# Optimization experiments

Measured on AMD Instinct MI355X. Metric: run time of the kernel, lower is better.

The kernel has to match this reference:

```python
import jax, jax.numpy as jnp
import numpy as np

B, L, V, A = 4096, 64, 50000, 1000
E, H, G, F2 = 32, 32, 256, 512


def _xavier(k, shape):
    fan_out, fan_in = shape
    a = np.sqrt(6.0 / (fan_in + fan_out)).astype(np.float32)
    return jax.random.uniform(k, shape, jnp.float32, -a, a)


def setup_inputs() -> dict:
    key = jax.random.key(0)
    ks = jax.random.split(key, 32)
    inp = {}
    inp["q"] = jax.random.randint(ks[0], (B, L), 0, V)
    for i in range(8):
        inp[f"sf{i}"] = jax.random.randint(ks[1 + i], (B, L), 0, V)
    inp["emb"] = _xavier(ks[9], (V, E))
    # torch LSTM weight layout: [4H, in] with gate order i,f,g,o; biases init to 0
    inp["q_Wih"] = _xavier(ks[10], (4 * H, E))
    inp["q_Whh"] = _xavier(ks[11], (4 * H, H))
    inp["q_b"] = jnp.zeros((4 * H,), jnp.float32)
    inp["sf_Wih"] = _xavier(ks[12], (4 * H, E))
    inp["sf_Whh"] = _xavier(ks[13], (4 * H, H))
    inp["sf_b"] = jnp.zeros((4 * H,), jnp.float32)
    inp["g1_W"] = _xavier(ks[14], (G, 2 * H + 1)); inp["g1_b"] = jnp.zeros((G,), jnp.float32)
    inp["g2_W"] = _xavier(ks[15], (G, G)); inp["g2_b"] = jnp.zeros((G,), jnp.float32)
    inp["g3_W"] = _xavier(ks[16], (G, G)); inp["g3_b"] = jnp.zeros((G,), jnp.float32)
    inp["g4_W"] = _xavier(ks[17], (G, G)); inp["g4_b"] = jnp.zeros((G,), jnp.float32)
    inp["f1_W"] = _xavier(ks[18], (G, G)); inp["f1_b"] = jnp.zeros((G,), jnp.float32)
    inp["f2_W"] = _xavier(ks[19], (F2, G)); inp["f2_b"] = jnp.zeros((F2,), jnp.float32)
    inp["f3_W"] = _xavier(ks[20], (A, F2)); inp["f3_b"] = jnp.zeros((A,), jnp.float32)
    return inp


def _lstm_last(x, Wih, Whh, b):
    """x: [L, N, E] -> final hidden state [N, H]. Torch gate order i,f,g,o."""
    n = x.shape[1]
    h_dim = Whh.shape[1]
    def step(carry, xt):
        h, c = carry
        gates = xt @ Wih.T + h @ Whh.T + b  # [N, 4H]
        i, f, g, o = jnp.split(gates, 4, axis=-1)
        c = jax.nn.sigmoid(f) * c + jax.nn.sigmoid(i) * jnp.tanh(g)
        h = jax.nn.sigmoid(o) * jnp.tanh(c)
        return (h, c), None
    init = (jnp.zeros((n, h_dim), x.dtype), jnp.zeros((n, h_dim), x.dtype))
    (h, _), _ = jax.lax.scan(step, init, x)
    return h


def _lin(x, W, b):
    return x @ W.T + b


def reference(q, sf0, sf1, sf2, sf3, sf4, sf5, sf6, sf7,
              emb, q_Wih, q_Whh, q_b, sf_Wih, sf_Whh, sf_b,
              g1_W, g1_b, g2_W, g2_b, g3_W, g3_b, g4_W, g4_b,
              f1_W, f1_b, f2_W, f2_b, f3_W, f3_b):
    # dropout in eval mode (identity)
    b, l = q.shape
    qe = emb[q].transpose(1, 0, 2)  # [L, B, E]
    hq = _lstm_last(qe, q_Wih, q_Whh, q_b)  # [B, H]

    sf = jnp.stack([sf0, sf1, sf2, sf3, sf4, sf5, sf6, sf7])  # [8, B, L]
    sfe = emb[sf]  # [8, B, L, E]
    sfe = sfe.transpose(2, 0, 1, 3).reshape(l, 8 * b, emb.shape[1])  # one fused LSTM over 8*B
    hs = _lstm_last(sfe, sf_Wih, sf_Whh, sf_b).reshape(8, b, -1)  # [8, B, H]

    pos = jnp.broadcast_to(jnp.arange(8, dtype=hs.dtype)[:, None, None], (8, b, 1))
    x = jnp.concatenate([hs, jnp.broadcast_to(hq, (8, b, hq.shape[-1])), pos], axis=-1)  # [8, B, 65]
    x = jax.nn.relu(_lin(x, g1_W, g1_b))
    x = jax.nn.relu(_lin(x, g2_W, g2_b))
    x = jax.nn.relu(_lin(x, g3_W, g3_b))
    x = jax.nn.relu(_lin(x, g4_W, g4_b))
    g_o = x.sum(axis=0)  # [B, 256] segment-sum over the 8 relations

    x = jax.nn.relu(_lin(g_o, f1_W, f1_b))
    x = jax.nn.relu(_lin(x, f2_W, f2_b))
    return _lin(x, f3_W, f3_b)  # [B, A]
```

## Files before the change

### kernel.cpp

```cpp
#include <hip/hip_runtime.h>
#include <stdint.h>
#include <stddef.h>

typedef __fp16 f16;
typedef __attribute__((ext_vector_type(8))) __fp16 half8;
typedef __attribute__((ext_vector_type(4))) float f32x4;

static __device__ __forceinline__ f32x4 mfma16(half8 a, half8 b, f32x4 c) {
    return __builtin_amdgcn_mfma_f32_16x16x32_f16(a, b, c, 0, 0, 0);
}
static __device__ __forceinline__ float fexp2(float x) { float r; asm("v_exp_f32 %0, %1" : "=v"(r) : "v"(x)); return r; }
static __device__ __forceinline__ float frcp(float x)  { float r; asm("v_rcp_f32 %0, %1" : "=v"(r) : "v"(x)); return r; }

static constexpr float L2E  = 1.4426950408889634f;
static constexpr float L2E2 = 2.8853900817779268f;

static constexpr size_t OFF_EMB   = 0;
static constexpr size_t OFF_WQIH  = 3200000;
static constexpr size_t OFF_WQHH  = OFF_WQIH + 8192;
static constexpr size_t OFF_WSIH  = OFF_WQHH + 8192;
static constexpr size_t OFF_WSHH  = OFF_WSIH + 8192;
static constexpr size_t OFF_BQ    = OFF_WSHH + 8192;
static constexpr size_t OFF_BS    = OFF_BQ + 512;
static constexpr size_t OFF_G1WP  = OFF_BS + 512;
static constexpr size_t OFF_BIAS8 = OFF_G1WP + 32768;
static constexpr size_t OFF_G2W   = OFF_BIAS8 + 8192;
static constexpr size_t OFF_G3W   = OFF_G2W + 131072;
static constexpr size_t OFF_G4W   = OFF_G3W + 131072;
static constexpr size_t OFF_F1W   = OFF_G4W + 131072;
static constexpr size_t OFF_F2W   = OFF_F1W + 131072;
static constexpr size_t OFF_F3W   = OFF_F2W + 262144;
static constexpr size_t OFF_HS    = OFF_F3W + 1024000;
static constexpr size_t OFF_HQ    = OFF_HS + 2097152;
static constexpr size_t OFF_ACT1  = OFF_HQ + 262144;
static constexpr size_t OFF_ACT2  = OFF_ACT1 + 16777216;
static constexpr size_t WS_NEED   = OFF_ACT2 + 16777216;
static constexpr size_t OFF_GO    = OFF_ACT1;
static constexpr size_t OFF_FA    = OFF_ACT1 + 2097152;
static constexpr size_t OFF_FB    = OFF_ACT1 + 4194304;

struct CvtJobs { const float* src[7]; f16* dst[7]; int n[7]; };

__global__ __launch_bounds__(256) void cvt_multi(CvtJobs j) {
    int t = blockIdx.y;
    int i = (blockIdx.x * 256 + threadIdx.x) * 8;
    if (i >= j.n[t]) return;
    const float* s = j.src[t] + i;
    f32x4 a = *(const f32x4*)s;
    f32x4 b = *(const f32x4*)(s + 4);
    half8 o;
    o[0]=(f16)a[0]; o[1]=(f16)a[1]; o[2]=(f16)a[2]; o[3]=(f16)a[3];
    o[4]=(f16)b[0]; o[5]=(f16)b[1]; o[6]=(f16)b[2]; o[7]=(f16)b[3];
    *(half8*)(j.dst[t] + i) = o;
}

__global__ __launch_bounds__(256) void prep_small(
    const float* __restrict__ g1W, const float* __restrict__ g1b,
    f16* __restrict__ wp, float* __restrict__ bias8,
    const float* __restrict__ qWih, const float* __restrict__ qWhh, const float* __restrict__ qb,
    const float* __restrict__ sWih, const float* __restrict__ sWhh, const float* __restrict__ sb,
    f16* __restrict__ wqih, f16* __restrict__ wqhh, float* __restrict__ bq,
    f16* __restrict__ wsih, f16* __restrict__ wshh, float* __restrict__ bs)
{
    int t = threadIdx.x;
    if (blockIdx.x == 0) {
        int col = t;
        for (int k = 0; k < 64; k++) wp[col * 64 + k] = (f16)g1W[col * 65 + k];
        float wpos = g1W[col * 65 + 64];
        float b = g1b[col];
        for (int i = 0; i < 8; i++) bias8[i * 256 + col] = b + (float)i * wpos;
    } else {
        for (int i = t; i < 4096; i += 256) {
            int row = i >> 5;
            float s = (row < 64 || row >= 96) ? -L2E : L2E2;
            wqih[i] = (f16)(qWih[i] * s);
            wqhh[i] = (f16)(qWhh[i] * s);
            wsih[i] = (f16)(sWih[i] * s);
            wshh[i] = (f16)(sWhh[i] * s);
        }
        if (t < 128) {
            float s = (t < 64 || t >= 96) ? -L2E : L2E2;
            bq[t] = qb[t] * s;
            bs[t] = sb[t] * s;
        }
    }
}

struct SfPtrs { const int* p[8]; };

__global__ __launch_bounds__(64) void lstm_kernel(
    SfPtrs sf, const int* __restrict__ qtok, const f16* __restrict__ emb_h,
    const f16* __restrict__ wih_sf, const f16* __restrict__ whh_sf, const float* __restrict__ b_sf,
    const f16* __restrict__ wih_q,  const f16* __restrict__ whh_q,  const float* __restrict__ b_q,
    f16* __restrict__ hs_out, f16* __restrict__ hq_out)
{
    __shared__ __align__(16) char hb[16 * 80];
    int lane = threadIdx.x;
    int c15 = lane & 15, kq = lane >> 4;
    int sbase = blockIdx.x * 16;
    bool isq = sbase >= 32768;
    const f16* wih = isq ? wih_q : wih_sf;
    const f16* whh = isq ? whh_q : whh_sf;
    const float* bvec = isq ? b_q : b_sf;

    half8 wi[8], wh[8];
    f32x4 bc[8];
    #pragma unroll
    for (int n = 0; n < 8; n++) {
        int col = n * 16 + c15;
        wi[n] = *(const half8*)(wih + col * 32 + kq * 8);
        wh[n] = *(const half8*)(whh + col * 32 + kq * 8);
        float b = bvec[col];
        bc[n][0] = b; bc[n][1] = b; bc[n][2] = b; bc[n][3] = b;
    }
    int sg = sbase + c15;
    const int* tp;
    if (isq) tp = qtok + (sg - 32768) * 64;
    else     tp = sf.p[sg >> 12] + (sg & 4095) * 64;

    f32x4 zro = {0.f, 0.f, 0.f, 0.f};
    *(f32x4*)(hb + lane * 16) = zro;
    if (lane < 16) *(f32x4*)(hb + 1024 + lane * 16) = zro;
    asm volatile("s_waitcnt lgkmcnt(0)" ::: "memory");

    float cst[4][2] = {};
    const char* hrd = hb + c15 * 80 + kq * 16;

    int tok = tp[0];
    half8 xf = *(const half8*)(emb_h + (size_t)tok * 32 + kq * 8);

    #pragma unroll 1
    for (int t = 0; t < 64; t++) {
        half8 hf = *(const half8*)hrd;
        f32x4 acc[8];
        #pragma unroll
        for (int n = 0; n < 8; n++) acc[n] = mfma16(xf, wi[n], bc[n]);
        #pragma unroll
        for (int n = 0; n < 8; n++) acc[n] = mfma16(hf, wh[n], acc[n]);
        if (t < 63) {
            int tk = tp[t + 1];
            xf = *(const half8*)(emb_h + (size_t)tk * 32 + kq * 8);
        }
        #pragma unroll
        for (int r = 0; r < 4; r++) {
            #pragma unroll
            for (int jh = 0; jh < 2; jh++) {
                float ei = fexp2(acc[0 + jh][r]);
                float ef = fexp2(acc[2 + jh][r]);
                float eg = fexp2(acc[4 + jh][r]);
                float eo = fexp2(acc[6 + jh][r]);
                float si  = frcp(1.f + ei);
                float sfv = frcp(1.f + ef);
                float so  = frcp(1.f + eo);
                float tg  = fmaf(-2.f, frcp(1.f + eg), 1.f);
                float cn  = fmaf(sfv, cst[r][jh], si * tg);
                cst[r][jh] = cn;
                float e2  = fexp2(cn * L2E2);
                float th  = fmaf(-2.f, frcp(1.f + e2), 1.f);
                float hn  = so * th;
                *(f16*)(hb + (kq * 4 + r) * 80 + (jh * 16 + c15) * 2) = (f16)hn;
            }
        }
        asm volatile("s_waitcnt lgkmcnt(0)" ::: "memory");
    }
    int row = lane >> 2, ch = lane & 3;
    half8 hv = *(const half8*)(hb + row * 80 + ch * 16);
    int so_ = sbase + row;
    if (isq) *(half8*)(hq_out + (size_t)(so_ - 32768) * 32 + ch * 8) = hv;
    else     *(half8*)(hs_out + (size_t)so_ * 32 + ch * 8) = hv;
}

__global__ __launch_bounds__(256) void gemm_g1(
    const f16* __restrict__ hs, const f16* __restrict__ hq,
    const f16* __restrict__ Wp, const float* __restrict__ bias8,
    f16* __restrict__ out)
{
    int wave = threadIdx.x >> 6, lane = threadIdx.x & 63;
    int c15 = lane & 15, kq = lane >> 4;
    int wm = wave >> 1, wn = wave & 1;
    int m0 = blockIdx.x * 128 + wm * 64;
    int n0 = blockIdx.y * 128 + wn * 64;
    const float* bias = bias8 + ((blockIdx.x * 128) >> 12) * 256;
    f32x4 zro = {0.f, 0.f, 0.f, 0.f};
    f32x4 acc[4][4];
    #pragma unroll
    for (int a = 0; a < 4; a++)
        #pragma unroll
        for (int b = 0; b < 4; b++) acc[a][b] = zro;

    half8 av[4], bv[4];
    #pragma unroll
    for (int fm = 0; fm < 4; fm++) av[fm] = *(const half8*)(hs + (size_t)(m0 + fm * 16 + c15) * 32 + kq * 8);
    #pragma unroll
    for (int fn = 0; fn < 4; fn++) bv[fn] = *(const half8*)(Wp + (size_t)(n0 + fn * 16 + c15) * 64 + kq * 8);
    #pragma unroll
    for (int fm = 0; fm < 4; fm++)
        #pragma unroll
        for (int fn = 0; fn < 4; fn++) acc[fm][fn] = mfma16(av[fm], bv[fn], acc[fm][fn]);
    #pragma unroll
    for (int fm = 0; fm < 4; fm++) av[fm] = *(const half8*)(hq + (size_t)((m0 + fm * 16 + c15) & 4095) * 32 + kq * 8);
    #pragma unroll
    for (int fn = 0; fn < 4; fn++) bv[fn] = *(const half8*)(Wp + (size_t)(n0 + fn * 16 + c15) * 64 + 32 + kq * 8);
    #pragma unroll
    for (int fm = 0; fm < 4; fm++)
        #pragma unroll
        for (int fn = 0; fn < 4; fn++) acc[fm][fn] = mfma16(av[fm], bv[fn], acc[fm][fn]);
    #pragma unroll
    for (int fn = 0; fn < 4; fn++) {
        int col = n0 + fn * 16 + c15;
        float bb = bias[col];
        #pragma unroll
        for (int fm = 0; fm < 4; fm++)
            #pragma unroll
            for (int r = 0; r < 4; r++) {
                int row = m0 + fm * 16 + kq * 4 + r;
                float v = acc[fm][fn][r] + bb;
                v = fmaxf(v, 0.f);
                out[(size_t)row * 256 + col] = (f16)v;
            }
    }
}

template<int K, bool RELU, bool OUTF32>
__global__ __launch_bounds__(256) void gemm_k(
    const f16* __restrict__ A, const f16* __restrict__ W, const float* __restrict__ bias,
    void* __restrict__ outv, int N, int ldout)
{
    int wave = threadIdx.x >> 6, lane = threadIdx.x & 63;
    int c15 = lane & 15, kq = lane >> 4;
    int wm = wave >> 1, wn = wave & 1;
    int m0 = blockIdx.x * 128 + wm * 64;
    int n0 = blockIdx.y * 128 + wn * 64;
    f32x4 zro = {0.f, 0.f, 0.f, 0.f};
    f32x4 acc[4][4];
    #pragma unroll
    for (int a = 0; a < 4; a++)
        #pragma unroll
        for (int b = 0; b < 4; b++) acc[a][b] = zro;

    const f16* ap[4];
    const f16* bp[4];
    #pragma unroll
    for (int fm = 0; fm < 4; fm++) ap[fm] = A + (size_t)(m0 + fm * 16 + c15) * K + kq * 8;
    #pragma unroll
    for (int fn = 0; fn < 4; fn++) {
        int col = n0 + fn * 16 + c15;
        if (col > N - 1) col = N - 1;
        bp[fn] = W + (size_t)col * K + kq * 8;
    }
    for (int k0 = 0; k0 < K; k0 += 32) {
        half8 av[4], bv[4];
        #pragma unroll
        for (int fm = 0; fm < 4; fm++) av[fm] = *(const half8*)(ap[fm] + k0);
        #pragma unroll
        for (int fn = 0; fn < 4; fn++) bv[fn] = *(const half8*)(bp[fn] + k0);
        #pragma unroll
        for (int fm = 0; fm < 4; fm++)
            #pragma unroll
            for (int fn = 0; fn < 4; fn++) acc[fm][fn] = mfma16(av[fm], bv[fn], acc[fm][fn]);
    }
    #pragma unroll
    for (int fn = 0; fn < 4; fn++) {
        int col = n0 + fn * 16 + c15;
        if (col < N) {
            float bb = bias[col];
            #pragma unroll
            for (int fm = 0; fm < 4; fm++)
                #pragma unroll
                for (int r = 0; r < 4; r++) {
                    int row = m0 + fm * 16 + kq * 4 + r;
                    float v = acc[fm][fn][r] + bb;
                    if (RELU) v = fmaxf(v, 0.f);
                    if (OUTF32) ((float*)outv)[(size_t)row * ldout + col] = v;
                    else ((f16*)outv)[(size_t)row * ldout + col] = (f16)v;
                }
        }
    }
}

__global__ __launch_bounds__(256) void sum8_kernel(const f16* __restrict__ g4o, f16* __restrict__ go) {
    int t = blockIdx.x * 256 + threadIdx.x;
    int b = t >> 5, chk = t & 31;
    const f16* p = g4o + (size_t)b * 256 + chk * 8;
    float a[8] = {};
    #pragma unroll
    for (int i = 0; i < 8; i++) {
        half8 v = *(const half8*)(p + (size_t)i * 4096 * 256);
        #pragma unroll
        for (int j = 0; j < 8; j++) a[j] += (float)v[j];
    }
    half8 o;
    #pragma unroll
    for (int j = 0; j < 8; j++) o[j] = (f16)a[j];
    *(half8*)(go + (size_t)b * 256 + chk * 8) = o;
}

extern "C" void kernel_launch(void* const* d_in, const int* in_sizes, int n_in,
                              void* d_out, int out_size, void* d_ws, size_t ws_size,
                              hipStream_t stream)
{
    if (ws_size < WS_NEED) return;
    const int* q_tok = (const int*)d_in[0];
    SfPtrs sf;
    for (int i = 0; i < 8; i++) sf.p[i] = (const int*)d_in[1 + i];
    const float* emb_f = (const float*)d_in[9];
    const float* qWih = (const float*)d_in[10];
    const float* qWhh = (const float*)d_in[11];
    const float* q_b  = (const float*)d_in[12];
    const float* sWih = (const float*)d_in[13];
    const float* sWhh = (const float*)d_in[14];
    const float* s_b  = (const float*)d_in[15];
    const float* g1W  = (const float*)d_in[16];
    const float* g1b  = (const float*)d_in[17];
    const float* g2W  = (const float*)d_in[18];
    const float* g2b  = (const float*)d_in[19];
    const float* g3W  = (const float*)d_in[20];
    const float* g3b  = (const float*)d_in[21];
    const float* g4W  = (const float*)d_in[22];
    const float* g4b  = (const float*)d_in[23];
    const float* f1W  = (const float*)d_in[24];
    const float* f1b  = (const float*)d_in[25];
    const float* f2W  = (const float*)d_in[26];
    const float* f2b  = (const float*)d_in[27];
    const float* f3W  = (const float*)d_in[28];
    const float* f3b  = (const float*)d_in[29];

    char* ws = (char*)d_ws;
    f16* emb_h = (f16*)(ws + OFF_EMB);
    f16* wqih  = (f16*)(ws + OFF_WQIH);
    f16* wqhh  = (f16*)(ws + OFF_WQHH);
    f16* wsih  = (f16*)(ws + OFF_WSIH);
    f16* wshh  = (f16*)(ws + OFF_WSHH);
    float* bq  = (float*)(ws + OFF_BQ);
    float* bs  = (float*)(ws + OFF_BS);
    f16* g1wp  = (f16*)(ws + OFF_G1WP);
    float* bias8 = (float*)(ws + OFF_BIAS8);
    f16* g2w = (f16*)(ws + OFF_G2W);
    f16* g3w = (f16*)(ws + OFF_G3W);
    f16* g4w = (f16*)(ws + OFF_G4W);
    f16* f1w = (f16*)(ws + OFF_F1W);
    f16* f2w = (f16*)(ws + OFF_F2W);
    f16* f3w = (f16*)(ws + OFF_F3W);
    f16* hs  = (f16*)(ws + OFF_HS);
    f16* hq  = (f16*)(ws + OFF_HQ);
    f16* act1 = (f16*)(ws + OFF_ACT1);
    f16* act2 = (f16*)(ws + OFF_ACT2);
    f16* go = (f16*)(ws + OFF_GO);
    f16* fa = (f16*)(ws + OFF_FA);
    f16* fb = (f16*)(ws + OFF_FB);

    CvtJobs cj;
    const float* srcs[7] = {emb_f, g2W, g3W, g4W, f1W, f2W, f3W};
    f16* dsts[7]         = {emb_h, g2w, g3w, g4w, f1w, f2w, f3w};
    int ns[7] = {1600000, 65536, 65536, 65536, 65536, 131072, 512000};
    for (int i = 0; i < 7; i++) { cj.src[i] = srcs[i]; cj.dst[i] = dsts[i]; cj.n[i] = ns[i]; }

    cvt_multi<<<dim3(782, 7), 256, 0, stream>>>(cj);
    prep_small<<<2, 256, 0, stream>>>(g1W, g1b, g1wp, bias8,
                                      qWih, qWhh, q_b, sWih, sWhh, s_b,
                                      wqih, wqhh, bq, wsih, wshh, bs);
    lstm_kernel<<<2304, 64, 0, stream>>>(sf, q_tok, emb_h, wsih, wshh, bs, wqih, wqhh, bq, hs, hq);
    gemm_g1<<<dim3(256, 2), 256, 0, stream>>>(hs, hq, g1wp, bias8, act1);
    gemm_k<256, true, false><<<dim3(256, 2), 256, 0, stream>>>(act1, g2w, g2b, act2, 256, 256);
    gemm_k<256, true, false><<<dim3(256, 2), 256, 0, stream>>>(act2, g3w, g3b, act1, 256, 256);
    gemm_k<256, true, false><<<dim3(256, 2), 256, 0, stream>>>(act1, g4w, g4b, act2, 256, 256);
    sum8_kernel<<<512, 256, 0, stream>>>(act2, go);
    gemm_k<256, true, false><<<dim3(32, 2), 256, 0, stream>>>(go, f1w, f1b, fa, 256, 256);
    gemm_k<256, true, false><<<dim3(32, 4), 256, 0, stream>>>(fa, f2w, f2b, fb, 512, 512);
    gemm_k<512, false, true><<<dim3(32, 8), 256, 0, stream>>>(fb, f3w, f3b, d_out, 1000, 1000);
}
```

Baseline: 373.3 us.

## Fuse MLP layers into two kernels, transpose LSTM MFMA, merge prep kernels

Merges the conversion and prep kernels into one launch. Fuses g1 through g4 into a single kernel that keeps activations in shared memory, and fuses the 8-way sum with f1, f2 and f3 into a second kernel. This removes several launches and the HBM round trips for intermediate activations. The LSTM swaps MFMA operand order so each lane writes a contiguous half4 of h, and it rewrites the gate math to use fewer reciprocals. It also drops the explicit LDS waitcnt barriers, which risks synchronization hazards, and the fused GEMMs use smaller tiles that reload weights from global memory per block.

```diff
diff --git a/kernel.cpp b/kernel.cpp
--- a/kernel.cpp
+++ b/kernel.cpp
@@ -4,6 +4,7 @@
 
 typedef __fp16 f16;
 typedef __attribute__((ext_vector_type(8))) __fp16 half8;
+typedef __attribute__((ext_vector_type(4))) __fp16 half4;
 typedef __attribute__((ext_vector_type(4))) float f32x4;
 
 static __device__ __forceinline__ f32x4 mfma16(half8 a, half8 b, f32x4 c) {
@@ -14,6 +15,9 @@
 
 static constexpr float L2E  = 1.4426950408889634f;
 static constexpr float L2E2 = 2.8853900817779268f;
+
+static constexpr int LD256 = 280;
+static constexpr int LD512 = 536;
 
 static constexpr size_t OFF_EMB   = 0;
 static constexpr size_t OFF_WQIH  = 3200000;
@@ -32,29 +36,13 @@
 static constexpr size_t OFF_F3W   = OFF_F2W + 262144;
 static constexpr size_t OFF_HS    = OFF_F3W + 1024000;
 static constexpr size_t OFF_HQ    = OFF_HS + 2097152;
-static constexpr size_t OFF_ACT1  = OFF_HQ + 262144;
-static constexpr size_t OFF_ACT2  = OFF_ACT1 + 16777216;
+static constexpr size_t OFF_ACT2  = OFF_HQ + 262144;
 static constexpr size_t WS_NEED   = OFF_ACT2 + 16777216;
-static constexpr size_t OFF_GO    = OFF_ACT1;
-static constexpr size_t OFF_FA    = OFF_ACT1 + 2097152;
-static constexpr size_t OFF_FB    = OFF_ACT1 + 4194304;
 
 struct CvtJobs { const float* src[7]; f16* dst[7]; int n[7]; };
 
-__global__ __launch_bounds__(256) void cvt_multi(CvtJobs j) {
-    int t = blockIdx.y;
-    int i = (blockIdx.x * 256 + threadIdx.x) * 8;
-    if (i >= j.n[t]) return;
-    const float* s = j.src[t] + i;
-    f32x4 a = *(const f32x4*)s;
-    f32x4 b = *(const f32x4*)(s + 4);
-    half8 o;
-    o[0]=(f16)a[0]; o[1]=(f16)a[1]; o[2]=(f16)a[2]; o[3]=(f16)a[3];
-    o[4]=(f16)b[0]; o[5]=(f16)b[1]; o[6]=(f16)b[2]; o[7]=(f16)b[3];
-    *(half8*)(j.dst[t] + i) = o;
-}
-
-__global__ __launch_bounds__(256) void prep_small(
+__global__ __launch_bounds__(256) void cvt_prep(
+    CvtJobs j,
     const float* __restrict__ g1W, const float* __restrict__ g1b,
     f16* __restrict__ wp, float* __restrict__ bias8,
     const float* __restrict__ qWih, const float* __restrict__ qWhh, const float* __restrict__ qb,
@@ -63,13 +51,26 @@
     f16* __restrict__ wsih, f16* __restrict__ wshh, float* __restrict__ bs)
 {
     int t = threadIdx.x;
+    if (blockIdx.y < 7) {
+        int jb = blockIdx.y;
+        int i = (blockIdx.x * 256 + t) * 8;
+        if (i >= j.n[jb]) return;
+        const float* s = j.src[jb] + i;
+        f32x4 a = *(const f32x4*)s;
+        f32x4 b = *(const f32x4*)(s + 4);
+        half8 o;
+        o[0]=(f16)a[0]; o[1]=(f16)a[1]; o[2]=(f16)a[2]; o[3]=(f16)a[3];
+        o[4]=(f16)b[0]; o[5]=(f16)b[1]; o[6]=(f16)b[2]; o[7]=(f16)b[3];
+        *(half8*)(j.dst[jb] + i) = o;
+        return;
+    }
     if (blockIdx.x == 0) {
         int col = t;
         for (int k = 0; k < 64; k++) wp[col * 64 + k] = (f16)g1W[col * 65 + k];
         float wpos = g1W[col * 65 + 64];
         float b = g1b[col];
         for (int i = 0; i < 8; i++) bias8[i * 256 + col] = b + (float)i * wpos;
-    } else {
+    } else if (blockIdx.x == 1) {
         for (int i = t; i < 4096; i += 256) {
             int row = i >> 5;
             float s = (row < 64 || row >= 96) ? -L2E : L2E2;
@@ -107,11 +108,9 @@
     f32x4 bc[8];
     #pragma unroll
     for (int n = 0; n < 8; n++) {
-        int col = n * 16 + c15;
-        wi[n] = *(const half8*)(wih + col * 32 + kq * 8);
-        wh[n] = *(const half8*)(whh + col * 32 + kq * 8);
-        float b = bvec[col];
-        bc[n][0] = b; bc[n][1] = b; bc[n][2] = b; bc[n][3] = b;
+        wi[n] = *(const half8*)(wih + (n * 16 + c15) * 32 + kq * 8);
+        wh[n] = *(const half8*)(whh + (n * 16 + c15) * 32 + kq * 8);
+        bc[n] = *(const f32x4*)(bvec + n * 16 + kq * 4);
     }
     int sg = sbase + c15;
     const int* tp;
@@ -121,9 +120,8 @@
     f32x4 zro = {0.f, 0.f, 0.f, 0.f};
     *(f32x4*)(hb + lane * 16) = zro;
     if (lane < 16) *(f32x4*)(hb + 1024 + lane * 16) = zro;
-    asm volatile("s_waitcnt lgkmcnt(0)" ::: "memory");
-
-    float cst[4][2] = {};
+
+    float cst[2][4] = {};
     const char* hrd = hb + c15 * 80 + kq * 16;
 
     int tok = tp[0];
@@ -134,165 +132,240 @@
         half8 hf = *(const half8*)hrd;
         f32x4 acc[8];
         #pragma unroll
-        for (int n = 0; n < 8; n++) acc[n] = mfma16(xf, wi[n], bc[n]);
-        #pragma unroll
-        for (int n = 0; n < 8; n++) acc[n] = mfma16(hf, wh[n], acc[n]);
+        for (int n = 0; n < 8; n++) acc[n] = mfma16(wi[n], xf, bc[n]);
+        #pragma unroll
+        for (int n = 0; n < 8; n++) acc[n] = mfma16(wh[n], hf, acc[n]);
         if (t < 63) {
             int tk = tp[t + 1];
             xf = *(const half8*)(emb_h + (size_t)tk * 32 + kq * 8);
         }
         #pragma unroll
-        for (int r = 0; r < 4; r++) {
-            #pragma unroll
-            for (int jh = 0; jh < 2; jh++) {
+        for (int jh = 0; jh < 2; jh++) {
+            half4 hp;
+            #pragma unroll
+            for (int r = 0; r < 4; r++) {
                 float ei = fexp2(acc[0 + jh][r]);
                 float ef = fexp2(acc[2 + jh][r]);
                 float eg = fexp2(acc[4 + jh][r]);
                 float eo = fexp2(acc[6 + jh][r]);
-                float si  = frcp(1.f + ei);
-                float sfv = frcp(1.f + ef);
-                float so  = frcp(1.f + eo);
-                float tg  = fmaf(-2.f, frcp(1.f + eg), 1.f);
-                float cn  = fmaf(sfv, cst[r][jh], si * tg);
-                cst[r][jh] = cn;
-                float e2  = fexp2(cn * L2E2);
-                float th  = fmaf(-2.f, frcp(1.f + e2), 1.f);
-                float hn  = so * th;
-                *(f16*)(hb + (kq * 4 + r) * 80 + (jh * 16 + c15) * 2) = (f16)hn;
-            }
-        }
-        asm volatile("s_waitcnt lgkmcnt(0)" ::: "memory");
-    }
-    int row = lane >> 2, ch = lane & 3;
-    half8 hv = *(const half8*)(hb + row * 80 + ch * 16);
-    int so_ = sbase + row;
-    if (isq) *(half8*)(hq_out + (size_t)(so_ - 32768) * 32 + ch * 8) = hv;
-    else     *(half8*)(hs_out + (size_t)so_ * 32 + ch * 8) = hv;
-}
-
-__global__ __launch_bounds__(256) void gemm_g1(
-    const f16* __restrict__ hs, const f16* __restrict__ hq,
-    const f16* __restrict__ Wp, const float* __restrict__ bias8,
-    f16* __restrict__ out)
-{
-    int wave = threadIdx.x >> 6, lane = threadIdx.x & 63;
-    int c15 = lane & 15, kq = lane >> 4;
-    int wm = wave >> 1, wn = wave & 1;
-    int m0 = blockIdx.x * 128 + wm * 64;
-    int n0 = blockIdx.y * 128 + wn * 64;
-    const float* bias = bias8 + ((blockIdx.x * 128) >> 12) * 256;
-    f32x4 zro = {0.f, 0.f, 0.f, 0.f};
-    f32x4 acc[4][4];
+                float t1 = 1.f + ei, t2 = 1.f + ef, t5 = 1.f + eo;
+                float eg1 = eg + 1.f, egm = eg - 1.f;
+                float num = fmaf(egm, t2, cst[jh][r] * t1 * eg1);
+                float den = (t2 * t1) * eg1;
+                float cn  = num * frcp(den);
+                cst[jh][r] = cn;
+                float ec  = fexp2(cn * L2E2);
+                float hv  = (ec - 1.f) * frcp((ec + 1.f) * t5);
+                hp[r] = (f16)hv;
+            }
+            *(half4*)(hb + c15 * 80 + jh * 32 + kq * 8) = hp;
+        }
+    }
+    half8 hv = *(const half8*)hrd;
+    if (isq) *(half8*)(hq_out + (size_t)(sg - 32768) * 32 + kq * 8) = hv;
+    else     *(half8*)(hs_out + (size_t)sg * 32 + kq * 8) = hv;
+}
+
+template<bool TOGLOBAL>
+static __device__ __forceinline__ void layer256(
+    const f16 (* __restrict__ src)[LD256], f16 (* __restrict__ dst)[LD256],
+    const f16* __restrict__ W, const float* __restrict__ bias,
+    f16* __restrict__ gout, int m0, int wv, int c15, int kq)
+{
+    f32x4 acc[2][4];
     #pragma unroll
-    for (int a = 0; a < 4; a++)
-        #pragma unroll
-        for (int b = 0; b < 4; b++) acc[a][b] = zro;
-
-    half8 av[4], bv[4];
+    for (int a = 0; a < 2; a++)
+        #pragma unroll
+        for (int b = 0; b < 4; b++) acc[a][b] = (f32x4){0.f, 0.f, 0.f, 0.f};
     #pragma unroll
-    for (int fm = 0; fm < 4; fm++) av[fm] = *(const half8*)(hs + (size_t)(m0 + fm * 16 + c15) * 32 + kq * 8);
-    #pragma unroll
-    for (int fn = 0; fn < 4; fn++) bv[fn] = *(const half8*)(Wp + (size_t)(n0 + fn * 16 + c15) * 64 + kq * 8);
-    #pragma unroll
-    for (int fm = 0; fm < 4; fm++)
-        #pragma unroll
-        for (int fn = 0; fn < 4; fn++) acc[fm][fn] = mfma16(av[fm], bv[fn], acc[fm][fn]);
-    #pragma unroll
-    for (int fm = 0; fm < 4; fm++) av[fm] = *(const half8*)(hq + (size_t)((m0 + fm * 16 + c15) & 4095) * 32 + kq * 8);
-    #pragma unroll
-    for (int fn = 0; fn < 4; fn++) bv[fn] = *(const half8*)(Wp + (size_t)(n0 + fn * 16 + c15) * 64 + 32 + kq * 8);
-    #pragma unroll
-    for (int fm = 0; fm < 4; fm++)
-        #pragma unroll
-        for (int fn = 0; fn < 4; fn++) acc[fm][fn] = mfma16(av[fm], bv[fn], acc[fm][fn]);
+    for (int k0 = 0; k0 < 8; k0++) {
+        half8 av[2], bv[4];
+        #pragma unroll
+        for (int fm = 0; fm < 2; fm++) av[fm] = *(const half8*)(&src[fm * 16 + c15][k0 * 32 + kq * 8]);
+        #pragma unroll
+        for (int fn = 0; fn < 4; fn++) bv[fn] = *(const half8*)(W + (size_t)(wv * 64 + fn * 16 + c15) * 256 + k0 * 32 + kq * 8);
+        #pragma unroll
+        for (int fm = 0; fm < 2; fm++)
+            #pragma unroll
+            for (int fn = 0; fn < 4; fn++) acc[fm][fn] = mfma16(av[fm], bv[fn], acc[fm][fn]);
+    }
     #pragma unroll
     for (int fn = 0; fn < 4; fn++) {
-        int col = n0 + fn * 16 + c15;
+        int col = wv * 64 + fn * 16 + c15;
         float bb = bias[col];
         #pragma unroll
-        for (int fm = 0; fm < 4; fm++)
+        for (int fm = 0; fm < 2; fm++)
             #pragma unroll
             for (int r = 0; r < 4; r++) {
-                int row = m0 + fm * 16 + kq * 4 + r;
-                float v = acc[fm][fn][r] + bb;
-                v = fmaxf(v, 0.f);
-                out[(size_t)row * 256 + col] = (f16)v;
-            }
-    }
-}
-
-template<int K, bool RELU, bool OUTF32>
-__global__ __launch_bounds__(256) void gemm_k(
-    const f16* __restrict__ A, const f16* __restrict__ W, const float* __restrict__ bias,
-    void* __restrict__ outv, int N, int ldout)
-{
-    int wave = threadIdx.x >> 6, lane = threadIdx.x & 63;
-    int c15 = lane & 15, kq = lane >> 4;
-    int wm = wave >> 1, wn = wave & 1;
-    int m0 = blockIdx.x * 128 + wm * 64;
-    int n0 = blockIdx.y * 128 + wn * 64;
-    f32x4 zro = {0.f, 0.f, 0.f, 0.f};
-    f32x4 acc[4][4];
-    #pragma unroll
-    for (int a = 0; a < 4; a++)
-        #pragma unroll
-        for (int b = 0; b < 4; b++) acc[a][b] = zro;
-
-    const f16* ap[4];
-    const f16* bp[4];
-    #pragma unroll
-    for (int fm = 0; fm < 4; fm++) ap[fm] = A + (size_t)(m0 + fm * 16 + c15) * K + kq * 8;
-    #pragma unroll
-    for (int fn = 0; fn < 4; fn++) {
-        int col = n0 + fn * 16 + c15;
-        if (col > N - 1) col = N - 1;
-        bp[fn] = W + (size_t)col * K + kq * 8;
-    }
-    for (int k0 = 0; k0 < K; k0 += 32) {
-        half8 av[4], bv[4];
-        #pragma unroll
-        for (int fm = 0; fm < 4; fm++) av[fm] = *(const half8*)(ap[fm] + k0);
-        #pragma unroll
-        for (int fn = 0; fn < 4; fn++) bv[fn] = *(const half8*)(bp[fn] + k0);
-        #pragma unroll
-        for (int fm = 0; fm < 4; fm++)
+                float v = fmaxf(acc[fm][fn][r] + bb, 0.f);
+                if (TOGLOBAL) gout[(size_t)(m0 + fm * 16 + kq * 4 + r) * 256 + col] = (f16)v;
+                else          dst[fm * 16 + kq * 4 + r][col] = (f16)v;
+            }
+    }
+}
+
+__global__ __launch_bounds__(256) void gemm_g1234(
+    const f16* __restrict__ hs, const f16* __restrict__ hq,
+    const f16* __restrict__ g1wp, const float* __restrict__ bias8,
+    const f16* __restrict__ g2w, const float* __restrict__ g2b,
+    const f16* __restrict__ g3w, const float* __restrict__ g3b,
+    const f16* __restrict__ g4w, const float* __restrict__ g4b,
+    f16* __restrict__ act2)
+{
+    __shared__ __align__(16) f16 actA[32][LD256];
+    __shared__ __align__(16) f16 actB[32][LD256];
+    const int wv = threadIdx.x >> 6, lane = threadIdx.x & 63;
+    const int c15 = lane & 15, kq = lane >> 4;
+    const int m0 = blockIdx.x * 32;
+    const float* brow = bias8 + ((m0 >> 12) << 8);
+
+    {
+        f32x4 acc[2][4];
+        #pragma unroll
+        for (int a = 0; a < 2; a++)
+            #pragma unroll
+            for (int b = 0; b < 4; b++) acc[a][b] = (f32x4){0.f, 0.f, 0.f, 0.f};
+        half8 av[2], bv[4];
+        #pragma unroll
+        for (int fm = 0; fm < 2; fm++) av[fm] = *(const half8*)(hs + (size_t)(m0 + fm * 16 + c15) * 32 + kq * 8);
+        #pragma unroll
+        for (int fn = 0; fn < 4; fn++) bv[fn] = *(const half8*)(g1wp + (size_t)(wv * 64 + fn * 16 + c15) * 64 + kq * 8);
+        #pragma unroll
+        for (int fm = 0; fm < 2; fm++)
             #pragma unroll
             for (int fn = 0; fn < 4; fn++) acc[fm][fn] = mfma16(av[fm], bv[fn], acc[fm][fn]);
-    }
-    #pragma unroll
-    for (int fn = 0; fn < 4; fn++) {
-        int col = n0 + fn * 16 + c15;
-        if (col < N) {
-            float bb = bias[col];
-            #pragma unroll
-            for (int fm = 0; fm < 4; fm++)
+        #pragma unroll
+        for (int fm = 0; fm < 2; fm++) av[fm] = *(const half8*)(hq + (size_t)((m0 + fm * 16 + c15) & 4095) * 32 + kq * 8);
+        #pragma unroll
+        for (int fn = 0; fn < 4; fn++) bv[fn] = *(const half8*)(g1wp + (size_t)(wv * 64 + fn * 16 + c15) * 64 + 32 + kq * 8);
+        #pragma unroll
+        for (int fm = 0; fm < 2; fm++)
+            #pragma unroll
+            for (int fn = 0; fn < 4; fn++) acc[fm][fn] = mfma16(av[fm], bv[fn], acc[fm][fn]);
+        #pragma unroll
+        for (int fn = 0; fn < 4; fn++) {
+            int col = wv * 64 + fn * 16 + c15;
+            float bb = brow[col];
+            #pragma unroll
+            for (int fm = 0; fm < 2; fm++)
                 #pragma unroll
-                for (int r = 0; r < 4; r++) {
-                    int row = m0 + fm * 16 + kq * 4 + r;
-                    float v = acc[fm][fn][r] + bb;
-                    if (RELU) v = fmaxf(v, 0.f);
-                    if (OUTF32) ((float*)outv)[(size_t)row * ldout + col] = v;
-                    else ((f16*)outv)[(size_t)row * ldout + col] = (f16)v;
-                }
-        }
-    }
-}
-
-__global__ __launch_bounds__(256) void sum8_kernel(const f16* __restrict__ g4o, f16* __restrict__ go) {
-    int t = blockIdx.x * 256 + threadIdx.x;
-    int b = t >> 5, chk = t & 31;
-    const f16* p = g4o + (size_t)b * 256 + chk * 8;
-    float a[8] = {};
-    #pragma unroll
-    for (int i = 0; i < 8; i++) {
-        half8 v = *(const half8*)(p + (size_t)i * 4096 * 256);
-        #pragma unroll
-        for (int j = 0; j < 8; j++) a[j] += (float)v[j];
-    }
-    half8 o;
-    #pragma unroll
-    for (int j = 0; j < 8; j++) o[j] = (f16)a[j];
-    *(half8*)(go + (size_t)b * 256 + chk * 8) = o;
+                for (int r = 0; r < 4; r++)
+                    actA[fm * 16 + kq * 4 + r][col] = (f16)fmaxf(acc[fm][fn][r] + bb, 0.f);
+        }
+    }
+    __syncthreads();
+    layer256<false>(actA, actB, g2w, g2b, nullptr, m0, wv, c15, kq);
+    __syncthreads();
+    layer256<false>(actB, actA, g3w, g3b, nullptr, m0, wv, c15, kq);
+    __syncthreads();
+    layer256<true>(actA, actB, g4w, g4b, act2, m0, wv, c15, kq);
+}
+
+__global__ __launch_bounds__(256) void f123s_kernel(
+    const f16* __restrict__ act2,
+    const f16* __restrict__ f1w, const float* __restrict__ f1b,
+    const f16* __restrict__ f2w, const float* __restrict__ f2b,
+    const f16* __restrict__ f3w, const float* __restrict__ f3b,
+    float* __restrict__ out)
+{
+    __shared__ __align__(16) f16 smbuf[16][LD256];
+    __shared__ __align__(16) f16 f1buf[16][LD256];
+    __shared__ __align__(16) f16 f2buf[16][LD512];
+    const int b0 = blockIdx.x * 16;
+
+    {
+        int r = threadIdx.x >> 4, cb = (threadIdx.x & 15) * 16;
+        float s[16] = {};
+        #pragma unroll
+        for (int i = 0; i < 8; i++) {
+            const f16* p = act2 + ((size_t)(i * 4096 + b0 + r)) * 256 + cb;
+            half8 v0 = *(const half8*)p;
+            half8 v1 = *(const half8*)(p + 8);
+            #pragma unroll
+            for (int q = 0; q < 8; q++) { s[q] += (float)v0[q]; s[8 + q] += (float)v1[q]; }
+        }
+        half8 o0, o1;
+        #pragma unroll
+        for (int q = 0; q < 8; q++) { o0[q] = (f16)s[q]; o1[q] = (f16)s[8 + q]; }
+        *(half8*)(&smbuf[r][cb]) = o0;
+        *(half8*)(&smbuf[r][cb + 8]) = o1;
+    }
+    __syncthreads();
+    const int wv = threadIdx.x >> 6, lane = threadIdx.x & 63;
+    const int c15 = lane & 15, kq = lane >> 4;
+
+    {
+        f32x4 acc[4];
+        #pragma unroll
+        for (int b = 0; b < 4; b++) acc[b] = (f32x4){0.f, 0.f, 0.f, 0.f};
+        #pragma unroll
+        for (int k0 = 0; k0 < 8; k0++) {
+            half8 a = *(const half8*)(&smbuf[c15][k0 * 32 + kq * 8]);
+            #pragma unroll
+            for (int fn = 0; fn < 4; fn++) {
+                half8 bv = *(const half8*)(f1w + (size_t)(wv * 64 + fn * 16 + c15) * 256 + k0 * 32 + kq * 8);
+                acc[fn] = mfma16(a, bv, acc[fn]);
+            }
+        }
+        #pragma unroll
+        for (int fn = 0; fn < 4; fn++) {
+            int col = wv * 64 + fn * 16 + c15;
+            float bb = f1b[col];
+            #pragma unroll
+            for (int r = 0; r < 4; r++)
+                f1buf[kq * 4 + r][col] = (f16)fmaxf(acc[fn][r] + bb, 0.f);
+        }
+    }
+    __syncthreads();
+    {
+        f32x4 acc[8];
+        #pragma unroll
+        for (int b = 0; b < 8; b++) acc[b] = (f32x4){0.f, 0.f, 0.f, 0.f};
+        #pragma unroll
+        for (int k0 = 0; k0 < 8; k0++) {
+            half8 a = *(const half8*)(&f1buf[c15][k0 * 32 + kq * 8]);
+            #pragma unroll
+            for (int fn = 0; fn < 8; fn++) {
+                half8 bv = *(const half8*)(f2w + (size_t)(wv * 128 + fn * 16 + c15) * 256 + k0 * 32 + kq * 8);
+                acc[fn] = mfma16(a, bv, acc[fn]);
+            }
+        }
+        #pragma unroll
+        for (int fn = 0; fn < 8; fn++) {
+            int col = wv * 128 + fn * 16 + c15;
+            float bb = f2b[col];
+            #pragma unroll
+            for (int r = 0; r < 4; r++)
+                f2buf[kq * 4 + r][col] = (f16)fmaxf(acc[fn][r] + bb, 0.f);
+        }
+    }
+    __syncthreads();
+    {
+        f32x4 acc[16];
+        #pragma unroll
+        for (int b = 0; b < 16; b++) acc[b] = (f32x4){0.f, 0.f, 0.f, 0.f};
+        #pragma unroll
+        for (int k0 = 0; k0 < 16; k0++) {
+            half8 a = *(const half8*)(&f2buf[c15][k0 * 32 + kq * 8]);
+            #pragma unroll
+            for (int jj = 0; jj < 16; jj++) {
+                int col = (wv + 4 * jj) * 16 + c15;
+                int cl = col < 1000 ? col : 999;
+                half8 bv = *(const half8*)(f3w + (size_t)cl * 512 + k0 * 32 + kq * 8);
+                acc[jj] = mfma16(a, bv, acc[jj]);
+            }
+        }
+        #pragma unroll
+        for (int jj = 0; jj < 16; jj++) {
+            int col = (wv + 4 * jj) * 16 + c15;
+            if (col < 1000) {
+                float bb = f3b[col];
+                #pragma unroll
+                for (int r = 0; r < 4; r++)
+                    out[(size_t)(b0 + kq * 4 + r) * 1000 + col] = acc[jj][r] + bb;
+            }
+        }
+    }
 }
 
 extern "C" void kernel_launch(void* const* d_in, const int* in_sizes, int n_in,
@@ -343,11 +416,7 @@
     f16* f3w = (f16*)(ws + OFF_F3W);
     f16* hs  = (f16*)(ws + OFF_HS);
     f16* hq  = (f16*)(ws + OFF_HQ);
-    f16* act1 = (f16*)(ws + OFF_ACT1);
     f16* act2 = (f16*)(ws + OFF_ACT2);
-    f16* go = (f16*)(ws + OFF_GO);
-    f16* fa = (f16*)(ws + OFF_FA);
-    f16* fb = (f16*)(ws + OFF_FB);
 
     CvtJobs cj;
     const float* srcs[7] = {emb_f, g2W, g3W, g4W, f1W, f2W, f3W};
@@ -355,17 +424,10 @@
     int ns[7] = {1600000, 65536, 65536, 65536, 65536, 131072, 512000};
     for (int i = 0; i < 7; i++) { cj.src[i] = srcs[i]; cj.dst[i] = dsts[i]; cj.n[i] = ns[i]; }
 
-    cvt_multi<<<dim3(782, 7), 256, 0, stream>>>(cj);
-    prep_small<<<2, 256, 0, stream>>>(g1W, g1b, g1wp, bias8,
-                                      qWih, qWhh, q_b, sWih, sWhh, s_b,
-                                      wqih, wqhh, bq, wsih, wshh, bs);
+    cvt_prep<<<dim3(782, 8), 256, 0, stream>>>(cj, g1W, g1b, g1wp, bias8,
+                                               qWih, qWhh, q_b, sWih, sWhh, s_b,
+                                               wqih, wqhh, bq, wsih, wshh, bs);
     lstm_kernel<<<2304, 64, 0, stream>>>(sf, q_tok, emb_h, wsih, wshh, bs, wqih, wqhh, bq, hs, hq);
-    gemm_g1<<<dim3(256, 2), 256, 0, stream>>>(hs, hq, g1wp, bias8, act1);
-    gemm_k<256, true, false><<<dim3(256, 2), 256, 0, stream>>>(act1, g2w, g2b, act2, 256, 256);
-    gemm_k<256, true, false><<<dim3(256, 2), 256, 0, stream>>>(act2, g3w, g3b, act1, 256, 256);
-    gemm_k<256, true, false><<<dim3(256, 2), 256, 0, stream>>>(act1, g4w, g4b, act2, 256, 256);
-    sum8_kernel<<<512, 256, 0, stream>>>(act2, go);
-    gemm_k<256, true, false><<<dim3(32, 2), 256, 0, stream>>>(go, f1w, f1b, fa, 256, 256);
-    gemm_k<256, true, false><<<dim3(32, 4), 256, 0, stream>>>(fa, f2w, f2b, fb, 512, 512);
-    gemm_k<512, false, true><<<dim3(32, 8), 256, 0, stream>>>(fb, f3w, f3b, d_out, 1000, 1000);
-}
+    gemm_g1234<<<1024, 256, 0, stream>>>(hs, hq, g1wp, bias8, g2w, g2b, g3w, g3b, g4w, g4b, act2);
+    f123s_kernel<<<256, 256, 0, stream>>>(act2, f1w, f1b, f2w, f2b, f3w, f3b, (float*)d_out);
+}
```

Result: no change. 380.6 us (+2.0%).
